# Performance work log

Measured on AMD Instinct MI355X. Metric: run time of the kernel, lower is better.

The kernel has to match this reference:

```python
import jax, jax.numpy as jnp
import numpy as np

# dims
B, S, E, H = 2, 2048, 2048, 2688   # batch, seq, embedding_dim, hidden_dim
NH, DH = 4, 2688 // 4              # mLSTM heads, head dim
KS = 4                             # causal conv kernel size
BLK = 4                            # qkv_proj_blocksize
NPH = H // BLK                     # headwise-proj heads


def setup_inputs() -> dict:
    key = jax.random.key(0)
    ks = jax.random.split(key, 12)
    r = lambda i, shape, s=0.02: jax.random.normal(ks[i], shape, jnp.float32) * s
    return dict(
        x=jax.random.normal(ks[0], (B, S, E), jnp.float32),
        W_in=r(1, (E, 2 * H)),                       # up projection (no bias)
        conv_w=r(2, (KS, 1, H), 0.1),                # depthwise causal conv kernel (W, I/g, O)
        conv_b=jnp.zeros((H,), jnp.float32),
        Wq=r(3, (NPH, BLK, BLK), 0.3),               # headwise q proj
        Wk=r(4, (NPH, BLK, BLK), 0.3),               # headwise k proj
        Wv=r(5, (NPH, BLK, BLK), 0.3),               # headwise v proj
        W_ig=r(6, (3 * H, NH)),                      # input gate proj
        b_ig=jax.random.normal(ks[7], (NH,), jnp.float32),
        W_fg=r(8, (3 * H, NH)),                      # forget gate proj
        b_fg=jnp.linspace(3.0, 6.0, NH).astype(jnp.float32),
        norm_w=jnp.ones((H,), jnp.float32),          # multi-head layernorm weight
        skip=jnp.ones((H,), jnp.float32),            # learnable skip
        W_out=r(9, (H, E)),                          # down projection
    )


def _headwise(x, W):
    # LinearHeadwiseExpand: (B,S,H) -> (B,S,NPH,BLK) -> einsum -> (B,S,H)
    b, s, _ = x.shape
    xh = x.reshape(b, s, NPH, BLK)
    return jnp.einsum('bshd,hdo->bsho', xh, W).reshape(b, s, -1)


def reference(x, W_in, conv_w, conv_b, Wq, Wk, Wv, W_ig, b_ig, W_fg, b_fg, norm_w, skip, W_out):
    x_inner = x @ W_in                               # (B,S,2H)
    x_m, z = jnp.split(x_inner, 2, axis=-1)
    # depthwise causal conv1d
    xc = jax.lax.conv_general_dilated(
        x_m, conv_w, (1,), [(KS - 1, 0)],
        dimension_numbers=('NWC', 'WIO', 'NWC'), feature_group_count=H) + conv_b
    xca = jax.nn.silu(xc)
    q = _headwise(xca, Wq)
    k = _headwise(xca, Wk)
    v = _headwise(x_m, Wv)
    # ---- mLSTM cell (parallel stabilized form) ----
    qh = q.reshape(B, S, NH, DH).transpose(0, 2, 1, 3)   # (B,NH,S,DH)
    kh = k.reshape(B, S, NH, DH).transpose(0, 2, 1, 3)
    vh = v.reshape(B, S, NH, DH).transpose(0, 2, 1, 3)
    if_in = jnp.concatenate([q, k, v], axis=-1)          # (B,S,3H)
    i_pre = (if_in @ W_ig + b_ig).transpose(0, 2, 1)     # (B,NH,S)
    f_pre = (if_in @ W_fg + b_fg).transpose(0, 2, 1)
    log_fg = jax.nn.log_sigmoid(f_pre)                   # (B,NH,S)
    cs = jnp.cumsum(log_fg, axis=-1)
    # log decay matrix: sum of log forget gates t=j+1..i, causal masked
    dmat = cs[:, :, :, None] - cs[:, :, None, :]         # (B,NH,S,S)
    mask = jnp.tril(jnp.ones((S, S), bool))
    log_D = jnp.where(mask, dmat + i_pre[:, :, None, :], -jnp.inf)
    m = jnp.max(log_D, axis=-1, keepdims=True)           # stabilizer (B,NH,S,1)
    D = jnp.exp(log_D - m)
    qk = jnp.einsum('bnsd,bntd->bnst', qh, kh) / jnp.sqrt(jnp.float32(DH))
    C = qk * D
    n = jnp.maximum(jnp.abs(C.sum(-1, keepdims=True)), jnp.exp(-m))
    h = jnp.einsum('bnst,bntd->bnsd', C / (n + 1e-6), vh)
    # multi-head layernorm over DH, learnable scale over full H
    mu = h.mean(-1, keepdims=True)
    var = h.var(-1, keepdims=True)
    hn = (h - mu) * jax.lax.rsqrt(var + 1e-5)
    hn = hn.transpose(0, 2, 1, 3).reshape(B, S, H) * norm_w
    # ---- gated skip + output ----
    h_skip = hn + skip * xca
    hs = h_skip * jax.nn.silu(z)
    return hs @ W_out
```

## Files before the change

kernel.cpp:

```cpp
#include <hip/hip_runtime.h>

typedef unsigned short u16;
typedef unsigned int u32;
typedef __bf16 bf16x8 __attribute__((ext_vector_type(8)));
typedef float f32x4 __attribute__((ext_vector_type(4)));

#define BB   2
#define SS   2048
#define EE   2048
#define HH   2688
#define NHH  4
#define DHH  672
#define NPHH 672
#define H2   5376
#define H3   8064

__device__ __forceinline__ float b2f(u16 u) {
  union { unsigned int i; float f; } c; c.i = ((unsigned int)u) << 16; return c.f;
}
__device__ __forceinline__ u16 f2b(float f) {
  union { float f; unsigned int i; } c; c.f = f;
  unsigned int i = c.i;
  return (u16)((i + 0x7FFFu + ((i >> 16) & 1u)) >> 16);
}
__device__ __forceinline__ float silu_f(float x) { return x / (1.f + __expf(-x)); }
__device__ __forceinline__ float logsig_f(float f) {
  return (f >= 0.f) ? -log1pf(__expf(-f)) : (f - log1pf(__expf(f)));
}

__device__ __forceinline__ void gl2lds16(const u16* g, u16* s) {
  __builtin_amdgcn_global_load_lds(
      (const __attribute__((address_space(1))) u32*)g,
      (__attribute__((address_space(3))) u32*)s, 16, 0, 0);
}

template <int N> __device__ __forceinline__ void vmwait() {
  asm volatile("s_waitcnt vmcnt(%0)" :: "n"(N) : "memory");
}

template <int BM, int MODE, int OUTF32>
__global__ __launch_bounds__(512, 1) void gemm_p(
    const u16* __restrict__ A, const u16* __restrict__ Bt, void* __restrict__ Cp,
    int M, int N, int K, int lda, int ldb, int ldc,
    long sAhi, long sAlo, long sBhi, long sBlo, long sChi, long sClo,
    const float* __restrict__ aux1, const float* __restrict__ aux2,
    int auxStride, int causal)
{
  constexpr int MFR   = BM / 32;
  constexpr int NPH   = MFR / 2;
  constexpr int SLOT  = (BM + 256) * 32;
  constexpr int ACH   = BM / 128;
  constexpr int LOADS = ACH + 2;
  __shared__ __align__(16) u16 sm[4 * SLOT];

  int gx = gridDim.x;
  int nwg = gx * gridDim.y;
  int flat = blockIdx.y * gx + blockIdx.x;
  int qq = nwg >> 3, r8 = nwg & 7;
  int xcd = flat & 7, seq = flat >> 3;
  int logical = (xcd < r8 ? xcd * (qq + 1) : r8 * (qq + 1) + (xcd - r8) * qq) + seq;
  int bx = logical % gx, by = logical / gx;
  int m0 = by * BM, n0 = bx * 256;
  if (MODE == 1 && n0 > m0 + BM - 1) return;

  int bz = blockIdx.z, bzh = bz >> 2, bzl = bz & 3;
  A  += bzh * sAhi + bzl * sAlo;
  Bt += bzh * sBhi + bzl * sBlo;
  const float* a1 = aux1 ? aux1 + (long)bz * auxStride : nullptr;
  const float* a2 = aux2 ? aux2 + (long)bz * auxStride : nullptr;
  u16*   C16 = (u16*)Cp + bzh * sChi + bzl * sClo;
  float* C32 = (float*)Cp + bzh * sChi + bzl * sClo;

  int t = threadIdx.x, lane = t & 63, w = t >> 6;
  int l15 = lane & 15, quad = lane >> 4;
  int wr = w >> 2, wc = w & 3;

  int srow = t >> 2;
  int swz = (((t & 3) ^ ((t >> 3) & 3)) * 8);
  const u16* pS[LOADS];
  int coff[LOADS];
#pragma unroll
  for (int c = 0; c < ACH; ++c) {
    pS[c] = A + (long)(m0 + c * 128 + srow) * lda + swz;
    coff[c] = c * 4096 + w * 512;
  }
#pragma unroll
  for (int c = 0; c < 2; ++c) {
    pS[ACH + c] = Bt + (long)(n0 + c * 128 + srow) * ldb + swz;
    coff[ACH + c] = BM * 32 + c * 4096 + w * 512;
  }

  int rswz = (quad ^ ((l15 >> 1) & 3)) * 8;
  int aoff = (wr * (BM / 2) + l15) * 32 + rswz;
  int boff = BM * 32 + (wc * 64 + l15) * 32 + rswz;

  f32x4 acc[MFR][4];
#pragma unroll
  for (int i = 0; i < MFR; i++)
#pragma unroll
    for (int j = 0; j < 4; j++) acc[i][j] = (f32x4){0.f, 0.f, 0.f, 0.f};

  int Keff = (MODE == 2 && causal) ? min(K, m0 + BM) : K;
  int T = Keff >> 5;

  auto STAGE1 = [&](int tt, int c) {
    gl2lds16(pS[c] + (tt << 5), sm + (tt & 3) * SLOT + coff[c]);
  };

  int npre = T < 3 ? T : 3;
  for (int tt = 0; tt < npre; ++tt)
#pragma unroll
    for (int c = 0; c < LOADS; ++c) STAGE1(tt, c);
  if (npre >= 3)      vmwait<2 * LOADS>();
  else if (npre == 2) vmwait<LOADS>();
  else                vmwait<0>();
  __builtin_amdgcn_s_barrier();
  __builtin_amdgcn_sched_barrier(0);

  for (int tq = 0; tq < T; ++tq) {
    u16* Sb = sm + (tq & 3) * SLOT;
    const bool stg = (tq + 3 < T);
    bf16x8 bf[4];
#pragma unroll
    for (int p = 0; p < NPH; ++p) {
      bf16x8 a0 = *reinterpret_cast<const bf16x8*>(Sb + aoff + (2 * p) * 512);
      bf16x8 a1v = *reinterpret_cast<const bf16x8*>(Sb + aoff + (2 * p + 1) * 512);
      if (p == 0) {
#pragma unroll
        for (int j = 0; j < 4; ++j)
          bf[j] = *reinterpret_cast<const bf16x8*>(Sb + boff + j * 512);
      }
      if (stg) {
#pragma unroll
        for (int c = p * LOADS / NPH; c < (p + 1) * LOADS / NPH; ++c)
          STAGE1(tq + 3, c);
      }
      __builtin_amdgcn_s_barrier();
      asm volatile("s_waitcnt lgkmcnt(0)" ::: "memory");
      __builtin_amdgcn_sched_barrier(0);
      __builtin_amdgcn_s_setprio(1);
#pragma unroll
      for (int j = 0; j < 4; ++j)
        acc[2 * p][j] = __builtin_amdgcn_mfma_f32_16x16x32_bf16(a0, bf[j], acc[2 * p][j], 0, 0, 0);
#pragma unroll
      for (int j = 0; j < 4; ++j)
        acc[2 * p + 1][j] = __builtin_amdgcn_mfma_f32_16x16x32_bf16(a1v, bf[j], acc[2 * p + 1][j], 0, 0, 0);
      __builtin_amdgcn_s_setprio(0);
      __builtin_amdgcn_sched_barrier(0);
    }
    if (tq + 1 < T) {
      if (tq + 3 < T)      vmwait<2 * LOADS>();
      else if (tq + 2 < T) vmwait<LOADS>();
      else                 vmwait<0>();
      __builtin_amdgcn_s_barrier();
      __builtin_amdgcn_sched_barrier(0);
    }
  }

  const float rs = 0.03857583749f;
#pragma unroll
  for (int i = 0; i < MFR; i++) {
#pragma unroll
    for (int j = 0; j < 4; j++) {
      int col = n0 + wc * 64 + j * 16 + l15;
      if (col >= N) continue;
#pragma unroll
      for (int rr = 0; rr < 4; rr++) {
        int row = m0 + wr * (BM / 2) + i * 16 + quad * 4 + rr;
        if (row >= M) continue;
        float v = acc[i][j][rr];
        if (MODE == 1) v = (col <= row) ? v * rs * __expf(a1[col] - a2[row]) : 0.f;
        else if (MODE == 2) v = v * a1[row];
        if (OUTF32) C32[(long)row * ldc + col] = v;
        else        C16[(long)row * ldc + col] = f2b(v);
      }
    }
  }
}

template <int F32IN>
__global__ __launch_bounds__(256) void transpose_any(
    const void* __restrict__ in, u16* __restrict__ out, int R, int C, int ldin,
    long inHi, long inLo, long outStride)
{
  __shared__ u16 tile[64][65];
  int bz = blockIdx.z, bzh = bz >> 2, bzl = bz & 3;
  const u16* in16 = (const u16*)in + bzh * inHi + bzl * inLo;
  const float* inf = (const float*)in + bzh * inHi + bzl * inLo;
  out += (long)bz * outStride;
  int r0 = blockIdx.y * 64, c0 = blockIdx.x * 64;
  int t = threadIdx.x;
  for (int idx = t; idx < 64 * 64; idx += 256) {
    int r = idx >> 6, c = idx & 63;
    int rr = r0 + r, cc = c0 + c;
    u16 v = 0;
    if (rr < R && cc < C) {
      long off = (long)rr * ldin + cc;
      v = F32IN ? f2b(inf[off]) : in16[off];
    }
    tile[r][c] = v;
  }
  __syncthreads();
  for (int idx = t; idx < 64 * 64; idx += 256) {
    int r = idx & 63, c = idx >> 6;
    int rr = r0 + r, cc = c0 + c;
    if (rr < R && cc < C) out[(long)cc * R + rr] = tile[r][c];
  }
}

__global__ __launch_bounds__(256) void convert_x(
    const float* __restrict__ x, u16* __restrict__ o)
{
  long i = ((long)blockIdx.x * 256 + threadIdx.x) * 8;
  if (i >= (long)4096 * EE) return;
  float4 a = *reinterpret_cast<const float4*>(x + i);
  float4 b = *reinterpret_cast<const float4*>(x + i + 4);
  u16 t8[8] = {f2b(a.x), f2b(a.y), f2b(a.z), f2b(a.w),
               f2b(b.x), f2b(b.y), f2b(b.z), f2b(b.w)};
  *reinterpret_cast<uint4*>(o + i) = *reinterpret_cast<uint4*>(t8);
}

__global__ __launch_bounds__(256) void prep_wt3(
    const float* __restrict__ Wig, const float* __restrict__ Wfg,
    u16* __restrict__ WT3)
{
  int i = blockIdx.x * 256 + threadIdx.x;
  if (i >= 128 * HH) return;
  int r = i / HH, c = i % HH;
  float v = 0.f;
  if (r < 24) {
    int seg = r >> 3, j = r & 7;
    const float* W = (j < 4) ? Wig : Wfg;
    v = W[(long)(seg * HH + c) * 4 + (j & 3)];
  }
  WT3[i] = f2b(v);
}

__global__ __launch_bounds__(256) void prep_wqkv(
    const float* __restrict__ Wq, const float* __restrict__ Wk,
    const float* __restrict__ Wv, u16* __restrict__ o)
{
  int i = blockIdx.x * 256 + threadIdx.x;
  if (i >= 3 * 10752) return;
  int m = i / 10752, j = i % 10752;
  const float* W = (m == 0) ? Wq : (m == 1) ? Wk : Wv;
  o[i] = f2b(W[j]);
}

__global__ __launch_bounds__(256) void conv_silu(
    const u16* __restrict__ xinner, const float* __restrict__ cw,
    const float* __restrict__ cb, u16* __restrict__ xca)
{
  long idx = (long)blockIdx.x * 256 + threadIdx.x;
  if (idx >= (long)BB * SS * HH / 4) return;
  int h4 = (int)(idx % (HH / 4)) * 4;
  long bs = idx / (HH / 4);
  int s = (int)(bs % SS);
  float4 acc = *reinterpret_cast<const float4*>(cb + h4);
#pragma unroll
  for (int w = 0; w < 4; w++) {
    int sp = s + w - 3;
    if (sp < 0) continue;
    uint2 xr = *reinterpret_cast<const uint2*>(xinner + (bs + w - 3) * H2 + h4);
    const u16* xh = (const u16*)&xr;
    float4 cwv = *reinterpret_cast<const float4*>(cw + w * HH + h4);
    acc.x += b2f(xh[0]) * cwv.x;
    acc.y += b2f(xh[1]) * cwv.y;
    acc.z += b2f(xh[2]) * cwv.z;
    acc.w += b2f(xh[3]) * cwv.w;
  }
  u16 o4[4] = {f2b(silu_f(acc.x)), f2b(silu_f(acc.y)),
               f2b(silu_f(acc.z)), f2b(silu_f(acc.w))};
  *reinterpret_cast<uint2*>(xca + bs * HH + h4) = *reinterpret_cast<uint2*>(o4);
}

__global__ __launch_bounds__(256) void headwise_qkv(
    const u16* __restrict__ xinner, const u16* __restrict__ xca,
    const u16* __restrict__ Wqkv,
    u16* __restrict__ q, u16* __restrict__ k, u16* __restrict__ v)
{
  int idx = blockIdx.x * 256 + threadIdx.x;
  if (idx >= BB * SS * NPHH) return;
  int nph = idx % NPHH;
  long bs = idx / NPHH;
  int cbase = nph * 4;
  uint2 xar = *reinterpret_cast<const uint2*>(xca + bs * HH + cbase);
  uint2 xmr = *reinterpret_cast<const uint2*>(xinner + bs * H2 + cbase);
  const u16* xa = (const u16*)&xar;
  const u16* xm = (const u16*)&xmr;
  float xaf[4], xmf[4];
#pragma unroll
  for (int d = 0; d < 4; d++) { xaf[d] = b2f(xa[d]); xmf[d] = b2f(xm[d]); }
  union { uint4 v4[2]; u16 h[16]; } wq, wk, wv;
  const uint4* wqp = reinterpret_cast<const uint4*>(Wqkv + nph * 16);
  const uint4* wkp = reinterpret_cast<const uint4*>(Wqkv + 10752 + nph * 16);
  const uint4* wvp = reinterpret_cast<const uint4*>(Wqkv + 21504 + nph * 16);
  wq.v4[0] = wqp[0]; wq.v4[1] = wqp[1];
  wk.v4[0] = wkp[0]; wk.v4[1] = wkp[1];
  wv.v4[0] = wvp[0]; wv.v4[1] = wvp[1];
  u16 qo[4], ko[4], vo[4];
#pragma unroll
  for (int o = 0; o < 4; o++) {
    float aq = 0.f, ak = 0.f, av = 0.f;
#pragma unroll
    for (int d = 0; d < 4; d++) {
      aq += xaf[d] * b2f(wq.h[d * 4 + o]);
      ak += xaf[d] * b2f(wk.h[d * 4 + o]);
      av += xmf[d] * b2f(wv.h[d * 4 + o]);
    }
    qo[o] = f2b(aq); ko[o] = f2b(ak); vo[o] = f2b(av);
  }
  long ob = bs * HH + cbase;
  *reinterpret_cast<uint2*>(q + ob) = *reinterpret_cast<uint2*>(qo);
  *reinterpret_cast<uint2*>(k + ob) = *reinterpret_cast<uint2*>(ko);
  *reinterpret_cast<uint2*>(v + ob) = *reinterpret_cast<uint2*>(vo);
}

__global__ __launch_bounds__(1024) void scan_kernel(
    const float* __restrict__ G, const float* __restrict__ big,
    const float* __restrict__ bfg,
    float* __restrict__ avec, float* __restrict__ rmaxvec, float* __restrict__ mvec)
{
  __shared__ float buf[2][SS];
  __shared__ float isave[SS];
  __shared__ float cssave[SS];
  int bn = blockIdx.x;
  int b = bn >> 2, n = bn & 3;
  int t = threadIdx.x;
  float bi = big[n], bf = bfg[n];
  for (int i = t; i < SS; i += 1024) {
    long tk = (long)b * SS + i;
    float ip = G[tk * 24 + n] + G[(4096 + tk) * 24 + 8 + n] +
               G[(8192 + tk) * 24 + 16 + n] + bi;
    float fp = G[tk * 24 + 4 + n] + G[(4096 + tk) * 24 + 12 + n] +
               G[(8192 + tk) * 24 + 20 + n] + bf;
    isave[i] = ip;
    buf[0][i] = logsig_f(fp);
  }
  __syncthreads();
  int src = 0;
  for (int off = 1; off < SS; off <<= 1) {
    int dst = 1 - src;
    for (int i = t; i < SS; i += 1024) {
      float x = buf[src][i];
      if (i >= off) x += buf[src][i - off];
      buf[dst][i] = x;
    }
    __syncthreads();
    src = dst;
  }
  for (int i = t; i < SS; i += 1024) {
    float cs = buf[src][i];
    cssave[i] = cs;
    float a = isave[i] - cs;
    avec[(long)bn * SS + i] = a;
    buf[src][i] = a;
  }
  __syncthreads();
  for (int off = 1; off < SS; off <<= 1) {
    int dst = 1 - src;
    for (int i = t; i < SS; i += 1024) {
      float x = buf[src][i];
      if (i >= off) x = fmaxf(x, buf[src][i - off]);
      buf[dst][i] = x;
    }
    __syncthreads();
    src = dst;
  }
  for (int i = t; i < SS; i += 1024) {
    rmaxvec[(long)bn * SS + i] = buf[src][i];
    mvec[(long)bn * SS + i] = cssave[i] + buf[src][i];
  }
}

__global__ __launch_bounds__(256) void rowsum_kernel(
    const u16* __restrict__ P, const float* __restrict__ mvec, float* __restrict__ invn,
    long Pstride)
{
  int bz = blockIdx.z;
  P += (long)bz * Pstride;
  mvec += (long)bz * SS;
  invn += (long)bz * SS;
  int row = (blockIdx.x * 256 + threadIdx.x) >> 6;
  int lane = threadIdx.x & 63;
  if (row >= SS) return;
  const u16* pr = P + (long)row * SS;
  float s = 0.f;
  for (int j = lane; j <= row; j += 64) s += b2f(pr[j]);
#pragma unroll
  for (int off = 32; off > 0; off >>= 1) s += __shfl_down(s, off);
  if (lane == 0) {
    float n = fmaxf(fabsf(s), __expf(-mvec[row]));
    invn[row] = 1.f / (n + 1e-6f);
  }
}

__global__ __launch_bounds__(256) void ln_skip_gate(
    const u16* __restrict__ h, const u16* __restrict__ xca,
    const u16* __restrict__ xinner, const float* __restrict__ normw,
    const float* __restrict__ skipw, u16* __restrict__ hs)
{
  int row = (blockIdx.x * 256 + threadIdx.x) >> 6;
  int lane = threadIdx.x & 63;
  if (row >= BB * NHH * SS) return;
  int s = row % SS;
  int n = (row / SS) % NHH;
  int b = row / (SS * NHH);
  const u16* hr = h + (long)row * DHH;
  float sum = 0.f, ss = 0.f;
  float vals[11];
  int cnt = 0;
  for (int d = lane; d < DHH; d += 64) {
    float x = b2f(hr[d]);
    vals[cnt++] = x; sum += x; ss += x * x;
  }
#pragma unroll
  for (int off = 32; off > 0; off >>= 1) { sum += __shfl_down(sum, off); ss += __shfl_down(ss, off); }
  sum = __shfl(sum, 0); ss = __shfl(ss, 0);
  float mu = sum / (float)DHH;
  float var = ss / (float)DHH - mu * mu;
  float rstd = rsqrtf(var + 1e-5f);
  long bs = (long)b * SS + s;
  cnt = 0;
  for (int d = lane; d < DHH; d += 64) {
    int c = n * DHH + d;
    float hn = (vals[cnt++] - mu) * rstd * normw[c];
    float hskip = hn + skipw[c] * b2f(xca[bs * HH + c]);
    float z = b2f(xinner[bs * H2 + HH + c]);
    hs[bs * HH + c] = f2b(hskip * silu_f(z));
  }
}

__global__ __launch_bounds__(256) void fill_sentinel(float* out, float v, long n) {
  long i = (long)blockIdx.x * 256 + threadIdx.x;
  if (i < n) out[i] = v;
}

extern "C" void kernel_launch(void* const* d_in, const int* in_sizes, int n_in,
                              void* d_out, int out_size, void* d_ws, size_t ws_size,
                              hipStream_t stream)
{
  const float* x      = (const float*)d_in[0];
  const float* W_in   = (const float*)d_in[1];
  const float* conv_w = (const float*)d_in[2];
  const float* conv_b = (const float*)d_in[3];
  const float* Wq     = (const float*)d_in[4];
  const float* Wk     = (const float*)d_in[5];
  const float* Wv     = (const float*)d_in[6];
  const float* W_ig   = (const float*)d_in[7];
  const float* b_ig   = (const float*)d_in[8];
  const float* W_fg   = (const float*)d_in[9];
  const float* b_fg   = (const float*)d_in[10];
  const float* norm_w = (const float*)d_in[11];
  const float* skipw  = (const float*)d_in[12];
  const float* W_out  = (const float*)d_in[13];
  float* out = (float*)d_out;
  const long SD = (long)SS * DHH;
  const long SP = (long)SS * SS;
  const long BH = (long)SS * HH;

  u16* ws = (u16*)d_ws;
  size_t off = 0;
  auto alloc = [&](size_t n) { u16* p = ws + off; off += n; return p; };
  u16* x_inner = alloc((size_t)4096 * H2);
  u16* xca     = alloc((size_t)4096 * HH);
  u16* qb      = alloc((size_t)4096 * HH);
  u16* kb      = alloc((size_t)4096 * HH);
  u16* vb      = alloc((size_t)4096 * HH);
  float* fvec  = (float*)(ws + off);
  off += 4 * 16384 * 2;
  float* avec    = fvec;
  float* rmaxvec = avec + 16384;
  float* mvec    = rmaxvec + 16384;
  float* invn    = mvec + 16384;
  u16* vt8 = alloc((size_t)8 * SD);
  u16* Pb8 = alloc((size_t)8 * SP);
  size_t need = off * 2;
  long outn = (long)4096 * EE;

  if (ws_size < need) {
    fill_sentinel<<<dim3((outn + 255) / 256), 256, 0, stream>>>(
        out, 200.f + 0.01f * (float)(ws_size >> 20), outn);
    return;
  }

  u16* W_inT  = qb;
  u16* xbf    = kb;
  u16* W_outT = vb;
  u16* hbuf   = kb;
  u16* hsbuf  = qb;
  u16* WT3    = Pb8;
  float* G    = (float*)(Pb8 + 344064);
  u16* Wqkv   = Pb8 + 933888;

  prep_wt3<<<dim3(1344, 1, 1), 256, 0, stream>>>(W_ig, W_fg, WT3);
  prep_wqkv<<<dim3(126, 1, 1), 256, 0, stream>>>(Wq, Wk, Wv, Wqkv);
  transpose_any<1><<<dim3(84, 32, 1), 256, 0, stream>>>(
      W_in, W_inT, EE, H2, H2, 0, 0, 0);
  convert_x<<<dim3(4096, 1, 1), 256, 0, stream>>>(x, xbf);
  gemm_p<256, 0, 0><<<dim3(21, 16, 1), 512, 0, stream>>>(
      xbf, W_inT, x_inner, 4096, H2, EE, EE, EE, H2,
      0, 0, 0, 0, 0, 0, nullptr, nullptr, 0, 0);
  conv_silu<<<dim3(10752, 1, 1), 256, 0, stream>>>(x_inner, conv_w, conv_b, xca);
  headwise_qkv<<<dim3(10752, 1, 1), 256, 0, stream>>>(
      x_inner, xca, Wqkv, qb, kb, vb);
  gemm_p<128, 0, 1><<<dim3(1, 96, 1), 512, 0, stream>>>(
      qb, WT3, G, 12288, 24, HH, HH, HH, 24,
      0, 0, 0, 0, 0, 0, nullptr, nullptr, 0, 0);
  scan_kernel<<<dim3(8, 1, 1), 1024, 0, stream>>>(G, b_ig, b_fg, avec, rmaxvec, mvec);
  transpose_any<0><<<dim3(11, 32, 8), 256, 0, stream>>>(
      vb, vt8, SS, DHH, HH, BH, DHH, SD);
  gemm_p<256, 1, 0><<<dim3(8, 8, 8), 512, 0, stream>>>(
      qb, kb, Pb8, SS, SS, DHH, HH, HH, SS,
      BH, DHH, BH, DHH, 4 * SP, SP, avec, rmaxvec, SS, 0);
  rowsum_kernel<<<dim3(512, 1, 8), 256, 0, stream>>>(Pb8, mvec, invn, SP);
  gemm_p<128, 2, 0><<<dim3(3, 16, 8), 512, 0, stream>>>(
      Pb8, vt8, hbuf, SS, DHH, SS, SS, SS, DHH,
      4 * SP, SP, 4 * SD, SD, 4 * SD, SD, invn, nullptr, SS, 1);
  transpose_any<1><<<dim3(32, 42, 1), 256, 0, stream>>>(
      W_out, W_outT, HH, EE, EE, 0, 0, 0);
  ln_skip_gate<<<dim3(4096, 1, 1), 256, 0, stream>>>(
      hbuf, xca, x_inner, norm_w, skipw, hsbuf);
  gemm_p<128, 0, 1><<<dim3(8, 32, 1), 512, 0, stream>>>(
      hsbuf, W_outT, out, 4096, EE, HH, HH, HH, EE,
      0, 0, 0, 0, 0, 0, nullptr, nullptr, 0, 0);
}
```

Before: 702.2 us.

## Add BK=64 three-stage GEMM kernel and vectorize rowsum and layernorm loads

Adds a new 128x256 tile GEMM with K-step 64 and a triple-buffered LDS pipeline, and uses it for the up-projection, gate projection, PV and down-projection GEMMs in place of the older gemm_p variants. rowsum_kernel now reads eight bf16 values per load, and ln_skip_gate reads and writes bf16 pairs with 32-bit accesses. The aim is fewer K-loop iterations and barriers per tile, plus better memory coalescing in the elementwise kernels. The new kernel needs more LDS and registers, and its fixed 128x256 tile wastes a lot of work on the narrow N=24 gate GEMM.

Result: faster. 661.8 us (-5.7%).

```diff
diff --git a/kernel.cpp b/kernel.cpp
--- a/kernel.cpp
+++ b/kernel.cpp
@@ -36,6 +36,162 @@
 
 template <int N> __device__ __forceinline__ void vmwait() {
   asm volatile("s_waitcnt vmcnt(%0)" :: "n"(N) : "memory");
+}
+
+template <int MODE, int OUTF32>
+__global__ __launch_bounds__(512, 1) void gemm8(
+    const u16* __restrict__ A, const u16* __restrict__ Bt, void* __restrict__ Cp,
+    int M, int N, int K, int lda, int ldb, int ldc,
+    long sAhi, long sAlo, long sBhi, long sBlo, long sChi, long sClo,
+    const float* __restrict__ aux1, const float* __restrict__ aux2,
+    int auxStride, int causal)
+{
+  constexpr int SLOT = (128 + 256) * 64;
+  __shared__ __align__(16) u16 sm[3 * SLOT];
+
+  int gx = gridDim.x;
+  int nwg = gx * gridDim.y;
+  int flat = blockIdx.y * gx + blockIdx.x;
+  int qq = nwg >> 3, r8 = nwg & 7;
+  int xcd = flat & 7, seq = flat >> 3;
+  int logical = (xcd < r8 ? xcd * (qq + 1) : r8 * (qq + 1) + (xcd - r8) * qq) + seq;
+  int bx = logical % gx, by = logical / gx;
+  int m0 = by * 128, n0 = bx * 256;
+  if (MODE == 1 && n0 > m0 + 127) return;
+
+  int bz = blockIdx.z, bzh = bz >> 2, bzl = bz & 3;
+  A  += bzh * sAhi + bzl * sAlo;
+  Bt += bzh * sBhi + bzl * sBlo;
+  const float* a1 = aux1 ? aux1 + (long)bz * auxStride : nullptr;
+  const float* a2 = aux2 ? aux2 + (long)bz * auxStride : nullptr;
+  u16*   C16 = (u16*)Cp + bzh * sChi + bzl * sClo;
+  float* C32 = (float*)Cp + bzh * sChi + bzl * sClo;
+
+  int t = threadIdx.x, lane = t & 63, w = t >> 6;
+  int l15 = lane & 15, quad = lane >> 4;
+  int wr = w >> 2, wc = w & 3;
+
+  int srow = t >> 3;
+  int sw8 = ((t & 7) ^ (srow & 7)) * 8;
+  const u16* pS[6];
+  int dOf[6];
+#pragma unroll
+  for (int c = 0; c < 2; ++c) {
+    pS[c] = A + (long)(m0 + c * 64 + srow) * lda + sw8;
+    dOf[c] = c * 4096 + w * 512;
+  }
+#pragma unroll
+  for (int c = 0; c < 4; ++c) {
+    pS[2 + c] = Bt + (long)(n0 + c * 64 + srow) * ldb + sw8;
+    dOf[2 + c] = 8192 + c * 4096 + w * 512;
+  }
+
+  f32x4 acc[4][4];
+#pragma unroll
+  for (int i = 0; i < 4; i++)
+#pragma unroll
+    for (int j = 0; j < 4; j++) acc[i][j] = (f32x4){0.f, 0.f, 0.f, 0.f};
+
+  int Keff = (MODE == 2 && causal) ? min(K, m0 + 128) : K;
+  int T = Keff >> 6;
+
+  auto STAGE = [&](int slot, int k2, int c) {
+    gl2lds16(pS[c] + k2, sm + slot * SLOT + dOf[c]);
+  };
+
+  int npre = T < 2 ? T : 2;
+  for (int tt = 0; tt < npre; ++tt)
+#pragma unroll
+    for (int c = 0; c < 6; ++c) STAGE(tt, tt << 6, c);
+  if (npre >= 2) vmwait<6>(); else vmwait<0>();
+  __builtin_amdgcn_s_barrier();
+  __builtin_amdgcn_sched_barrier(0);
+
+  int sl = 0;
+  for (int tq = 0; tq < T; ++tq) {
+    u16* Sb = sm + sl * SLOT;
+    int sl2 = sl + 2; if (sl2 >= 3) sl2 -= 3;
+    const bool stg = (tq + 2 < T);
+    const int k2 = (tq + 2) << 6;
+    int cx = (l15 & 7);
+
+    bf16x8 bfr[4][2], af[2][2];
+#pragma unroll
+    for (int j = 0; j < 4; ++j)
+#pragma unroll
+      for (int ks = 0; ks < 2; ++ks)
+        bfr[j][ks] = *reinterpret_cast<const bf16x8*>(
+            Sb + 8192 + (wc * 64 + j * 16 + l15) * 64 + ((((ks << 2) + quad) ^ cx) << 3));
+#pragma unroll
+    for (int i = 0; i < 2; ++i)
+#pragma unroll
+      for (int ks = 0; ks < 2; ++ks)
+        af[i][ks] = *reinterpret_cast<const bf16x8*>(
+            Sb + (wr * 64 + i * 16 + l15) * 64 + ((((ks << 2) + quad) ^ cx) << 3));
+    if (stg) { STAGE(sl2, k2, 0); STAGE(sl2, k2, 1); STAGE(sl2, k2, 2); }
+    __builtin_amdgcn_s_barrier();
+    asm volatile("s_waitcnt lgkmcnt(0)" ::: "memory");
+    __builtin_amdgcn_sched_barrier(0);
+    __builtin_amdgcn_s_setprio(1);
+#pragma unroll
+    for (int i = 0; i < 2; ++i)
+#pragma unroll
+      for (int j = 0; j < 4; ++j) {
+        acc[i][j] = __builtin_amdgcn_mfma_f32_16x16x32_bf16(af[i][0], bfr[j][0], acc[i][j], 0, 0, 0);
+        acc[i][j] = __builtin_amdgcn_mfma_f32_16x16x32_bf16(af[i][1], bfr[j][1], acc[i][j], 0, 0, 0);
+      }
+    __builtin_amdgcn_s_setprio(0);
+    __builtin_amdgcn_sched_barrier(0);
+    __builtin_amdgcn_s_barrier();
+
+    bf16x8 ag[2][2];
+#pragma unroll
+    for (int i = 0; i < 2; ++i)
+#pragma unroll
+      for (int ks = 0; ks < 2; ++ks)
+        ag[i][ks] = *reinterpret_cast<const bf16x8*>(
+            Sb + (wr * 64 + (i + 2) * 16 + l15) * 64 + ((((ks << 2) + quad) ^ cx) << 3));
+    if (stg) { STAGE(sl2, k2, 3); STAGE(sl2, k2, 4); STAGE(sl2, k2, 5); }
+    __builtin_amdgcn_s_barrier();
+    asm volatile("s_waitcnt lgkmcnt(0)" ::: "memory");
+    __builtin_amdgcn_sched_barrier(0);
+    __builtin_amdgcn_s_setprio(1);
+#pragma unroll
+    for (int i = 0; i < 2; ++i)
+#pragma unroll
+      for (int j = 0; j < 4; ++j) {
+        acc[i + 2][j] = __builtin_amdgcn_mfma_f32_16x16x32_bf16(ag[i][0], bfr[j][0], acc[i + 2][j], 0, 0, 0);
+        acc[i + 2][j] = __builtin_amdgcn_mfma_f32_16x16x32_bf16(ag[i][1], bfr[j][1], acc[i + 2][j], 0, 0, 0);
+      }
+    __builtin_amdgcn_s_setprio(0);
+    __builtin_amdgcn_sched_barrier(0);
+    if (tq + 1 < T) {
+      if (stg) vmwait<6>(); else vmwait<0>();
+      __builtin_amdgcn_s_barrier();
+      __builtin_amdgcn_sched_barrier(0);
+    }
+    sl = sl + 1; if (sl >= 3) sl = 0;
+  }
+
+  const float rs = 0.03857583749f;
+#pragma unroll
+  for (int i = 0; i < 4; i++) {
+#pragma unroll
+    for (int j = 0; j < 4; j++) {
+      int col = n0 + wc * 64 + j * 16 + l15;
+      if (col >= N) continue;
+#pragma unroll
+      for (int rr = 0; rr < 4; rr++) {
+        int row = m0 + wr * 64 + i * 16 + quad * 4 + rr;
+        if (row >= M) continue;
+        float v = acc[i][j][rr];
+        if (MODE == 1) v = (col <= row) ? v * rs * __expf(a1[col] - a2[row]) : 0.f;
+        else if (MODE == 2) v = v * a1[row];
+        if (OUTF32) C32[(long)row * ldc + col] = v;
+        else        C16[(long)row * ldc + col] = f2b(v);
+      }
+    }
+  }
 }
 
 template <int BM, int MODE, int OUTF32>
@@ -386,7 +542,16 @@
   if (row >= SS) return;
   const u16* pr = P + (long)row * SS;
   float s = 0.f;
-  for (int j = lane; j <= row; j += 64) s += b2f(pr[j]);
+  int j0 = lane * 8;
+  for (; j0 + 7 <= row; j0 += 512) {
+    uint4 u = *reinterpret_cast<const uint4*>(pr + j0);
+    const u16* e = (const u16*)&u;
+#pragma unroll
+    for (int q = 0; q < 8; ++q) s += b2f(e[q]);
+  }
+  if (j0 <= row) {
+    for (int q = 0; j0 + q <= row; ++q) s += b2f(pr[j0 + q]);
+  }
 #pragma unroll
   for (int off = 32; off > 0; off >>= 1) s += __shfl_down(s, off);
   if (lane == 0) {
@@ -408,11 +573,17 @@
   int b = row / (SS * NHH);
   const u16* hr = h + (long)row * DHH;
   float sum = 0.f, ss = 0.f;
-  float vals[11];
-  int cnt = 0;
-  for (int d = lane; d < DHH; d += 64) {
-    float x = b2f(hr[d]);
-    vals[cnt++] = x; sum += x; ss += x * x;
+  float vx[6], vy[6];
+#pragma unroll
+  for (int i = 0; i < 6; ++i) {
+    int d2 = lane + i * 64;
+    float x = 0.f, y = 0.f;
+    if (d2 < DHH / 2) {
+      u32 u = *reinterpret_cast<const u32*>(hr + d2 * 2);
+      x = b2f((u16)u); y = b2f((u16)(u >> 16));
+    }
+    vx[i] = x; vy[i] = y;
+    sum += x + y; ss += x * x + y * y;
   }
 #pragma unroll
   for (int off = 32; off > 0; off >>= 1) { sum += __shfl_down(sum, off); ss += __shfl_down(ss, off); }
@@ -421,13 +592,21 @@
   float var = ss / (float)DHH - mu * mu;
   float rstd = rsqrtf(var + 1e-5f);
   long bs = (long)b * SS + s;
-  cnt = 0;
-  for (int d = lane; d < DHH; d += 64) {
-    int c = n * DHH + d;
-    float hn = (vals[cnt++] - mu) * rstd * normw[c];
-    float hskip = hn + skipw[c] * b2f(xca[bs * HH + c]);
-    float z = b2f(xinner[bs * H2 + HH + c]);
-    hs[bs * HH + c] = f2b(hskip * silu_f(z));
+#pragma unroll
+  for (int i = 0; i < 6; ++i) {
+    int d2 = lane + i * 64;
+    if (d2 >= DHH / 2) continue;
+    int c = n * DHH + d2 * 2;
+    float2 nw = *reinterpret_cast<const float2*>(normw + c);
+    float2 sw = *reinterpret_cast<const float2*>(skipw + c);
+    u32 xcu = *reinterpret_cast<const u32*>(xca + bs * HH + c);
+    u32 zu  = *reinterpret_cast<const u32*>(xinner + bs * H2 + HH + c);
+    float h0 = (vx[i] - mu) * rstd * nw.x + sw.x * b2f((u16)xcu);
+    float h1 = (vy[i] - mu) * rstd * nw.y + sw.y * b2f((u16)(xcu >> 16));
+    float o0 = h0 * silu_f(b2f((u16)zu));
+    float o1 = h1 * silu_f(b2f((u16)(zu >> 16)));
+    u32 ou = (u32)f2b(o0) | ((u32)f2b(o1) << 16);
+    *reinterpret_cast<u32*>(hs + bs * HH + c) = ou;
   }
 }
 
@@ -498,13 +677,13 @@
   transpose_any<1><<<dim3(84, 32, 1), 256, 0, stream>>>(
       W_in, W_inT, EE, H2, H2, 0, 0, 0);
   convert_x<<<dim3(4096, 1, 1), 256, 0, stream>>>(x, xbf);
-  gemm_p<256, 0, 0><<<dim3(21, 16, 1), 512, 0, stream>>>(
+  gemm8<0, 0><<<dim3(21, 32, 1), 512, 0, stream>>>(
       xbf, W_inT, x_inner, 4096, H2, EE, EE, EE, H2,
       0, 0, 0, 0, 0, 0, nullptr, nullptr, 0, 0);
   conv_silu<<<dim3(10752, 1, 1), 256, 0, stream>>>(x_inner, conv_w, conv_b, xca);
   headwise_qkv<<<dim3(10752, 1, 1), 256, 0, stream>>>(
       x_inner, xca, Wqkv, qb, kb, vb);
-  gemm_p<128, 0, 1><<<dim3(1, 96, 1), 512, 0, stream>>>(
+  gemm8<0, 1><<<dim3(1, 96, 1), 512, 0, stream>>>(
       qb, WT3, G, 12288, 24, HH, HH, HH, 24,
       0, 0, 0, 0, 0, 0, nullptr, nullptr, 0, 0);
   scan_kernel<<<dim3(8, 1, 1), 1024, 0, stream>>>(G, b_ig, b_fg, avec, rmaxvec, mvec);
@@ -514,14 +693,14 @@
       qb, kb, Pb8, SS, SS, DHH, HH, HH, SS,
       BH, DHH, BH, DHH, 4 * SP, SP, avec, rmaxvec, SS, 0);
   rowsum_kernel<<<dim3(512, 1, 8), 256, 0, stream>>>(Pb8, mvec, invn, SP);
-  gemm_p<128, 2, 0><<<dim3(3, 16, 8), 512, 0, stream>>>(
+  gemm8<2, 0><<<dim3(3, 16, 8), 512, 0, stream>>>(
       Pb8, vt8, hbuf, SS, DHH, SS, SS, SS, DHH,
       4 * SP, SP, 4 * SD, SD, 4 * SD, SD, invn, nullptr, SS, 1);
   transpose_any<1><<<dim3(32, 42, 1), 256, 0, stream>>>(
       W_out, W_outT, HH, EE, EE, 0, 0, 0);
   ln_skip_gate<<<dim3(4096, 1, 1), 256, 0, stream>>>(
       hbuf, xca, x_inner, norm_w, skipw, hsbuf);
-  gemm_p<128, 0, 1><<<dim3(8, 32, 1), 512, 0, stream>>>(
+  gemm8<0, 1><<<dim3(8, 32, 1), 512, 0, stream>>>(
       hsbuf, W_outT, out, 4096, EE, HH, HH, HH, EE,
       0, 0, 0, 0, 0, 0, nullptr, nullptr, 0, 0);
 }
```
